# Kernel tuning notes

Measured on AMD Instinct MI355X. Metric: run time of the kernel, lower is better.

The kernel has to match this reference:

```python
import jax, jax.numpy as jnp
import numpy as np


def _conv1x1(x, w, b=None):
    # x: [B,C,H,W], w: [O,C]
    y = jnp.einsum('bchw,oc->bohw', x, w)
    if b is not None:
        y = y + b[None, :, None, None]
    return y


def _conv3x3_dilated(x, w, b, dil):
    p = dil  # padding == dilation keeps spatial size for 3x3 kernels
    y = jax.lax.conv_general_dilated(
        x, w, window_strides=(1, 1), padding=((p, p), (p, p)),
        rhs_dilation=(dil, dil), dimension_numbers=('NCHW', 'OIHW', 'NCHW'))
    return y + b[None, :, None, None]


def _upsample2x_align_corners(x):
    # bilinear, align_corners=True, scale factor 2
    B, C, H, W = x.shape
    oh, ow = 2 * H, 2 * W
    ys = jnp.linspace(0.0, H - 1.0, oh)
    xs = jnp.linspace(0.0, W - 1.0, ow)
    y0 = jnp.floor(ys).astype(jnp.int32)
    x0 = jnp.floor(xs).astype(jnp.int32)
    y1 = jnp.minimum(y0 + 1, H - 1)
    x1 = jnp.minimum(x0 + 1, W - 1)
    wy = (ys - y0)[None, None, :, None]
    wx = (xs - x0)[None, None, None, :]
    gt = x[:, :, y0, :]
    gb = x[:, :, y1, :]
    top = gt[:, :, :, x0] * (1 - wx) + gt[:, :, :, x1] * wx
    bot = gb[:, :, :, x0] * (1 - wx) + gb[:, :, :, x1] * wx
    return top * (1 - wy) + bot * wy


def _gr(ftr, ck_w, ck_b, avg_w, max_w, gcn_w):
    # GR module: attention-diagonal graph conv with degree normalization
    B, C, H, W = ftr.shape
    HW = H * W
    # ChannelAttention_diag -> diagonal entries cw: [B, M]
    avg = ftr.mean(axis=(2, 3))
    mx = ftr.max(axis=(2, 3))
    cw = jax.nn.sigmoid(jax.nn.relu(avg @ avg_w.T) + jax.nn.relu(mx @ max_w.T))  # [B,M]
    k = jax.nn.relu(_conv1x1(ftr, ck_w, ck_b)).reshape(B, -1, HW)  # [B,M,HW]
    q = jnp.swapaxes(k, 1, 2)  # [B,HW,M]
    # A = sigmoid(q @ diag(cw) @ k); degree d = rowsum(A)^(-1/2)
    A = jax.nn.sigmoid(jnp.einsum('bim,bm,bmj->bij', q, cw, k))  # [B,HW,HW]
    d = A.sum(axis=2) ** -0.5  # [B,HW]
    P = d[:, :, None] * q  # D^{-1/2} @ q, [B,HW,M]
    X = jnp.swapaxes(ftr.reshape(B, C, HW), 1, 2)  # [B,HW,C]
    PtX = jnp.einsum('bjm,bjc->bmc', P, X)  # [B,M,C]
    LX = X - jnp.einsum('bim,bmc->bic', P, cw[:, :, None] * PtX)
    Y = X + LX @ gcn_w  # GCN (no bias)
    return jnp.swapaxes(Y, 1, 2).reshape(B, C, H, W)


def setup_inputs() -> dict:
    key = jax.random.key(0)
    ks = jax.random.split(key, 20)
    B, C = 64, 1024
    Cq = C // 4  # 256
    Mi = Cq // 2  # 128, ChannelAttention inter channels
    s = 0.02
    inp = {
        'x_cur': jax.random.normal(ks[0], (B, C, 16, 16), jnp.float32),
        'x_lat': jax.random.normal(ks[1], (B, C, 8, 8), jnp.float32),
        'conv_w': jax.random.normal(ks[2], (Cq, C), jnp.float32) * s,
        'conv_b': jax.random.normal(ks[3], (Cq,), jnp.float32) * s,
        'conv1_w': jax.random.normal(ks[4], (C, Cq), jnp.float32) * s,
        'conv1_b': jax.random.normal(ks[5], (C,), jnp.float32) * s,
        'conv3_w': jax.random.normal(ks[6], (C, 3 * Cq), jnp.float32) * s,
        'conv3_b': jax.random.normal(ks[7], (C,), jnp.float32) * s,
        'rate0_w': jax.random.normal(ks[8], (Cq, C, 3, 3), jnp.float32) * s,
        'rate0_b': jax.random.normal(ks[9], (Cq,), jnp.float32) * s,
        'rate1_w': jax.random.normal(ks[10], (Cq, C, 3, 3), jnp.float32) * s,
        'rate1_b': jax.random.normal(ks[11], (Cq,), jnp.float32) * s,
        'rate2_w': jax.random.normal(ks[12], (Cq, C, 3, 3), jnp.float32) * s,
        'rate2_b': jax.random.normal(ks[13], (Cq,), jnp.float32) * s,
        'gr_ck_w': jax.random.normal(ks[14], (Mi, Cq), jnp.float32) * s,
        'gr_ck_b': jax.random.normal(ks[15], (Mi,), jnp.float32) * s,
        'gr_avg_w': jax.random.normal(ks[16], (Mi, Cq), jnp.float32) * s,
        'gr_max_w': jax.random.normal(ks[17], (Mi, Cq), jnp.float32) * s,
        'gr_gcn_w': jax.random.normal(ks[18], (Cq, Cq), jnp.float32) * s,
        'pre': 1,
    }
    return inp


def reference(x_cur, x_lat, conv_w, conv_b, conv1_w, conv1_b, conv3_w, conv3_b,
              rate0_w, rate0_b, rate1_w, rate1_b, rate2_w, rate2_b,
              gr_ck_w, gr_ck_b, gr_avg_w, gr_max_w, gr_gcn_w, pre):
    # pre == 1 path of Graph_aspp.forward
    gr_args = (gr_ck_w, gr_ck_b, gr_avg_w, gr_max_w, gr_gcn_w)
    x_sum = x_cur * _upsample2x_align_corners(x_lat) + x_cur
    f1 = _conv3x3_dilated(x_sum, rate0_w, rate0_b, 1) + _conv1x1(x_sum, conv_w, conv_b)
    x1 = _gr(f1, *gr_args)
    feature = _conv1x1(f1, conv1_w, conv1_b) + x_sum
    f2 = _conv3x3_dilated(feature, rate1_w, rate1_b, 2) + _conv1x1(feature, conv_w, conv_b)
    x2 = _gr(f2, *gr_args)
    feature = _conv1x1(f2, conv1_w, conv1_b) + x_sum
    f3 = _conv3x3_dilated(feature, rate2_w, rate2_b, 4) + _conv1x1(feature, conv_w, conv_b)
    x3 = _gr(f3, *gr_args)
    cat = jnp.concatenate((x1, x2, x3), axis=1)
    return _conv1x1(cat, conv3_w, conv3_b)
```

## Files before the change

### kernel.cpp

```cpp
#include <hip/hip_runtime.h>


typedef unsigned short ushort_t;
typedef unsigned int uint32;
typedef __attribute__((ext_vector_type(8))) unsigned short ushort8;
typedef __attribute__((ext_vector_type(8))) __bf16 bf16x8;
typedef __attribute__((ext_vector_type(4))) float f32x4;

__device__ __forceinline__ ushort_t f2b(float f) {
    union { float f; uint32 u; } v; v.f = f;
    uint32 r = v.u + 0x7fffu + ((v.u >> 16) & 1u);
    return (ushort_t)(r >> 16);
}
__device__ __forceinline__ float b2f(ushort_t b) {
    union { uint32 u; float f; } v; v.u = ((uint32)b) << 16;
    return v.f;
}
__device__ __forceinline__ float sigm(float x) { return 1.f / (1.f + __expf(-x)); }

__device__ __forceinline__ void gload_lds16(const void* g, void* l) {
    __builtin_amdgcn_global_load_lds(
        (__attribute__((address_space(1))) void*)g,
        (__attribute__((address_space(3))) void*)l, 16, 0, 0);
}

constexpr int EPI_RELU  = 1;
constexpr int EPI_FQ    = 2;
constexpr int EPI_SIG   = 3;
constexpr int EPI_XG    = 4;
constexpr int EPI_NEGCW = 5;
constexpr int EPI_Y     = 6;
constexpr int EPI_OUTT  = 7;

struct GemmP {
    const ushort_t* A; const ushort_t* B;
    const ushort_t* A2; const ushort_t* B2;
    long long aBatch, bBatch, a2Batch, b2Batch;
    int lda, ldb, lda2, ldb2;
    int Ksub, kSplit, dil;
    const float* bias;
    const ushort_t* res; long long resBatch; int ldres;
    ushort_t* obf; long long oBatch; int ldo;
    ushort_t* obf2;
    float* of32;
    const float* cw;
    const float* rscale;
    float* dsum;
    const ushort_t* zpage;
};

__device__ __forceinline__ void big_body(ushort_t* aT, ushort_t* bT,
                                         const GemmP& p, int bx, int by, int z) {
    const int tid = threadIdx.x;
    const int m0 = bx * 128, n0 = by * 128;
    const int lane = tid & 63, wid = tid >> 6;
    const int l15 = lane & 15, l16 = lane >> 4;
    const int wr = wid >> 1, wc = wid & 1;
    const int lrow = lane >> 3;
    const int sgran = (lane & 7) ^ lrow;

    int ayy[4], axx[4];
    const ushort_t* aBase[4];
    const ushort_t* bBase[4];
#pragma unroll
    for (int i = 0; i < 4; ++i) {
        int row = wid * 32 + i * 8 + lrow;
        int m = m0 + row;
        int bb = m >> 8;
        ayy[i] = (m >> 4) & 15; axx[i] = m & 15;
        aBase[i] = p.A + (long long)bb * 262144 + sgran * 8;
        bBase[i] = p.B + (long long)(n0 + row) * p.ldb + sgran * 8;
    }

    f32x4 acc[4][4];
#pragma unroll
    for (int i = 0; i < 4; ++i)
#pragma unroll
        for (int j = 0; j < 4; ++j) acc[i][j] = (f32x4){0.f, 0.f, 0.f, 0.f};

    const int gk0 = z * p.kSplit;
    const int ntap = p.Ksub >> 10;
    for (int ti = 0; ti < ntap; ++ti) {
        const int tap = (gk0 >> 10) + ti;
        int dy = 0, dx = 0;
        if (tap < 9) { int ky = tap / 3; dy = (ky - 1) * p.dil; dx = (tap - ky * 3 - 1) * p.dil; }
        const ushort_t* gaA[4];
        const ushort_t* gaB[4];
#pragma unroll
        for (int i = 0; i < 4; ++i) {
            int iy = ayy[i] + dy, ix = axx[i] + dx;
            bool ok = ((unsigned)iy < 16u) && ((unsigned)ix < 16u);
            gaA[i] = ok ? (aBase[i] + (((iy << 4) + ix) << 10)) : (p.zpage + sgran * 8);
            gaB[i] = bBase[i] + (tap << 10);
        }
        for (int kk = 0; kk < 16; ++kk) {
            const int kin = kk << 6;
#pragma unroll
            for (int i = 0; i < 4; ++i)
                gload_lds16(gaA[i] + kin, &aT[(wid * 32 + i * 8) * 64]);
#pragma unroll
            for (int i = 0; i < 4; ++i)
                gload_lds16(gaB[i] + kin, &bT[(wid * 32 + i * 8) * 64]);
            asm volatile("s_waitcnt vmcnt(0)" ::: "memory");
            __syncthreads();
#pragma unroll
            for (int ks = 0; ks < 2; ++ks) {
                bf16x8 af[4], bfr[4];
#pragma unroll
                for (int mi = 0; mi < 4; ++mi) {
                    int rr = wr * 64 + mi * 16 + l15;
                    int cc = (ks * 32 + l16 * 8) ^ ((rr & 7) << 3);
                    af[mi] = __builtin_bit_cast(bf16x8, *(const ushort8*)&aT[rr * 64 + cc]);
                }
#pragma unroll
                for (int ni = 0; ni < 4; ++ni) {
                    int rr = wc * 64 + ni * 16 + l15;
                    int cc = (ks * 32 + l16 * 8) ^ ((rr & 7) << 3);
                    bfr[ni] = __builtin_bit_cast(bf16x8, *(const ushort8*)&bT[rr * 64 + cc]);
                }
#pragma unroll
                for (int mi = 0; mi < 4; ++mi)
#pragma unroll
                    for (int ni = 0; ni < 4; ++ni)
                        acc[mi][ni] = __builtin_amdgcn_mfma_f32_16x16x32_bf16(af[mi], bfr[ni], acc[mi][ni], 0, 0, 0);
            }
            __syncthreads();
        }
    }
#pragma unroll
    for (int mi = 0; mi < 4; ++mi)
#pragma unroll
        for (int ni = 0; ni < 4; ++ni) {
            int gcol = n0 + wc * 64 + ni * 16 + l15;
            int growb = m0 + wr * 64 + mi * 16 + l16 * 4;
#pragma unroll
            for (int r = 0; r < 4; ++r)
                p.obf[(long long)z * p.oBatch + (long long)(growb + r) * 256 + gcol] =
                    f2b(acc[mi][ni][r]);
        }
}

template<int BM, int BN, int AMODE, int EPI>
__device__ __forceinline__ void gemm_body(ushort_t* aT, ushort_t* bT,
                                          const GemmP& p, int bx, int by, int z) {
    constexpr int APASS = BM / 32, BPASS = BN / 32;
    constexpr int MFRAG = BM / 32, NFRAG = BN / 32;
    const int tid = threadIdx.x;
    const int m0 = bx * BM, n0 = by * BN;
    const int lane = tid & 63, wid = tid >> 6;
    const int l15 = lane & 15, l16 = lane >> 4;
    const int wr = wid >> 1, wc = wid & 1;
    const int srow = tid >> 3, scol = (tid & 7) * 8;
    const int swcol = scol ^ ((srow & 7) << 3);

    const ushort_t* aptr[APASS];
    const ushort_t* bptr[BPASS];
    const ushort_t* aptr2[APASS];
    const ushort_t* bptr2[BPASS];
    float rsA[APASS];
#pragma unroll
    for (int pi = 0; pi < APASS; ++pi)
        aptr[pi] = p.A + (long long)z * p.aBatch +
                   (long long)(m0 + pi * 32 + srow) * p.lda + scol;
#pragma unroll
    for (int pi = 0; pi < BPASS; ++pi)
        bptr[pi] = p.B + (long long)z * p.bBatch +
                   (long long)(n0 + pi * 32 + srow) * p.ldb + scol;
    if constexpr (AMODE == 2) {
#pragma unroll
        for (int pi = 0; pi < APASS; ++pi) {
            aptr2[pi] = p.A2 + (long long)z * p.a2Batch +
                        (long long)(m0 + pi * 32 + srow) * p.lda2 + scol;
            rsA[pi] = p.rscale[z * 256 + m0 + pi * 32 + srow];
        }
#pragma unroll
        for (int pi = 0; pi < BPASS; ++pi)
            bptr2[pi] = p.B2 + (long long)z * p.b2Batch +
                        (long long)(n0 + pi * 32 + srow) * p.ldb2 + scol;
    }

    f32x4 acc[MFRAG][NFRAG];
#pragma unroll
    for (int i = 0; i < MFRAG; ++i)
#pragma unroll
        for (int j = 0; j < NFRAG; ++j) acc[i][j] = (f32x4){0.f, 0.f, 0.f, 0.f};

    ushort8 ar[APASS], br[BPASS];
    auto ldg = [&](int gk) {
        if (AMODE == 2 && gk >= 256) {
            int g2 = gk - 256;
#pragma unroll
            for (int pi = 0; pi < APASS; ++pi) {
                ushort8 t8 = *(const ushort8*)(aptr2[pi] + g2);
#pragma unroll
                for (int k = 0; k < 8; ++k) t8[k] = f2b(b2f(t8[k]) * rsA[pi]);
                ar[pi] = t8;
            }
#pragma unroll
            for (int pi = 0; pi < BPASS; ++pi) br[pi] = *(const ushort8*)(bptr2[pi] + g2);
        } else if constexpr (AMODE == 3) {
#pragma unroll
            for (int pi = 0; pi < APASS; ++pi) {
                ushort8 t8 = *(const ushort8*)(aptr[pi] + gk);
#pragma unroll
                for (int k = 0; k < 8; ++k)
                    t8[k] = f2b(b2f(t8[k]) * p.cw[(z << 7) + gk + scol + k]);
                ar[pi] = t8;
            }
#pragma unroll
            for (int pi = 0; pi < BPASS; ++pi) br[pi] = *(const ushort8*)(bptr[pi] + gk);
        } else {
#pragma unroll
            for (int pi = 0; pi < APASS; ++pi) ar[pi] = *(const ushort8*)(aptr[pi] + gk);
#pragma unroll
            for (int pi = 0; pi < BPASS; ++pi) br[pi] = *(const ushort8*)(bptr[pi] + gk);
        }
    };

    const int gk0 = z * p.kSplit;
    ldg(gk0);
    const int iters = p.Ksub >> 6;
    for (int it = 0; it < iters; ++it) {
#pragma unroll
        for (int pi = 0; pi < APASS; ++pi)
            *(ushort8*)&aT[(pi * 32 + srow) * 64 + swcol] = ar[pi];
#pragma unroll
        for (int pi = 0; pi < BPASS; ++pi)
            *(ushort8*)&bT[(pi * 32 + srow) * 64 + swcol] = br[pi];
        __syncthreads();
        if (it + 1 < iters) ldg(gk0 + (it + 1) * 64);
#pragma unroll
        for (int ks = 0; ks < 2; ++ks) {
            bf16x8 af[MFRAG], bfr[NFRAG];
#pragma unroll
            for (int mi = 0; mi < MFRAG; ++mi) {
                int rr = wr * (BM / 2) + mi * 16 + l15;
                int cc = (ks * 32 + l16 * 8) ^ ((rr & 7) << 3);
                af[mi] = __builtin_bit_cast(bf16x8, *(const ushort8*)&aT[rr * 64 + cc]);
            }
#pragma unroll
            for (int ni = 0; ni < NFRAG; ++ni) {
                int rr = wc * (BN / 2) + ni * 16 + l15;
                int cc = (ks * 32 + l16 * 8) ^ ((rr & 7) << 3);
                bfr[ni] = __builtin_bit_cast(bf16x8, *(const ushort8*)&bT[rr * 64 + cc]);
            }
#pragma unroll
            for (int mi = 0; mi < MFRAG; ++mi)
#pragma unroll
                for (int ni = 0; ni < NFRAG; ++ni)
                    acc[mi][ni] = __builtin_amdgcn_mfma_f32_16x16x32_bf16(af[mi], bfr[ni], acc[mi][ni], 0, 0, 0);
        }
        __syncthreads();
    }

#pragma unroll
    for (int mi = 0; mi < MFRAG; ++mi) {
        if constexpr (EPI == EPI_SIG) {
#pragma unroll
            for (int r = 0; r < 4; ++r) {
                float sv = 0.f;
#pragma unroll
                for (int ni = 0; ni < NFRAG; ++ni) sv += sigm(acc[mi][ni][r]);
                sv += __shfl_xor(sv, 1); sv += __shfl_xor(sv, 2);
                sv += __shfl_xor(sv, 4); sv += __shfl_xor(sv, 8);
                if (l15 == 0) {
                    int grow = m0 + wr * (BM / 2) + mi * 16 + l16 * 4 + r;
                    int q8 = by * 2 + wc;
                    p.dsum[q8 * 16384 + z * 256 + grow] = sv;
                }
            }
        } else {
#pragma unroll
            for (int ni = 0; ni < NFRAG; ++ni) {
                int gcol = n0 + wc * (BN / 2) + ni * 16 + l15;
                int growb = m0 + wr * (BM / 2) + mi * 16 + l16 * 4;
#pragma unroll
                for (int r = 0; r < 4; ++r) {
                    int grow = growb + r;
                    float v = acc[mi][ni][r];
                    if constexpr (EPI == EPI_RELU) {
                        v += p.bias[gcol]; v = fmaxf(v, 0.f);
                        p.obf[(long long)grow * p.ldo + gcol] = f2b(v);
                    } else if constexpr (EPI == EPI_FQ) {
                        v += p.bias[gcol];
                        if (gcol < 1024) {
                            v += b2f(p.res[(long long)grow * 1024 + gcol]);
                            p.obf[(long long)grow * 1024 + gcol] = f2b(v);
                        } else {
                            v = fmaxf(v, 0.f);
                            p.obf2[(long long)grow * 128 + (gcol - 1024)] = f2b(v);
                        }
                    } else if constexpr (EPI == EPI_XG) {
                        p.obf[(long long)z * p.oBatch + (long long)grow * p.ldo + gcol] = f2b(v);
                    } else if constexpr (EPI == EPI_NEGCW) {
                        v *= -p.cw[z * 128 + gcol];
                        p.obf[(long long)z * p.oBatch + (long long)grow * p.ldo + gcol] = f2b(v);
                    } else if constexpr (EPI == EPI_Y) {
                        v = b2f(p.res[(long long)z * p.resBatch + (long long)grow * p.ldres + gcol]) + v;
                        p.obf[(long long)z * p.oBatch + (long long)grow * p.ldo + gcol] = f2b(v);
                    } else if constexpr (EPI == EPI_OUTT) {
                        v += p.bias[grow];
                        int bb = gcol >> 8, px = gcol & 255;
                        p.of32[((long long)bb * 1024 + grow) * 256 + px] = v;
                    }
                }
            }
        }
    }
}

template<int BM, int BN, int AMODE, int EPI>
__global__ __launch_bounds__(256) void gemm_k(GemmP p) {
    __shared__ __align__(16) ushort_t aT[BM * 64];
    __shared__ __align__(16) ushort_t bT[BN * 64];
    gemm_body<BM, BN, AMODE, EPI>(aT, bT, p, blockIdx.x, blockIdx.y, blockIdx.z);
}

__device__ __forceinline__ void pool_body(void* lds, int b, const ushort_t* f,
                                          const float* aw, const float* mw,
                                          float* cw) {
    float* sa = (float*)lds;
    float* sm = sa + 256;
    int t = threadIdx.x;
    float s = 0.f, m = -3.4e38f;
    const ushort_t* base = f + (long long)b * 65536 + t;
    for (int px = 0; px < 256; ++px) { float v = b2f(base[px * 256]); s += v; m = fmaxf(m, v); }
    sa[t] = s * (1.f / 256.f);
    sm[t] = m;
    __syncthreads();
    if (t < 128) {
        float s1 = 0.f, s2 = 0.f;
        const float* a = aw + t * 256; const float* w = mw + t * 256;
        for (int c = 0; c < 256; ++c) { s1 += sa[c] * a[c]; s2 += sm[c] * w[c]; }
        s1 = fmaxf(s1, 0.f); s2 = fmaxf(s2, 0.f);
        cw[b * 128 + t] = sigm(s1 + s2);
    }
}

__device__ __forceinline__ void pscale_body(int jh, int b,
                                            const ushort_t* q, const float* dsum8,
                                            float* dscale, ushort_t* Pt) {
    __shared__ ushort_t t[128][130];
    __shared__ float dd[128];
    int j0 = jh * 128;
    int tid = threadIdx.x;
    if (tid < 128) {
        int pix = b * 256 + j0 + tid;
        float s = 0.f;
#pragma unroll
        for (int qs = 0; qs < 8; ++qs) s += dsum8[qs * 16384 + pix];
        float r = rsqrtf(s);
        dd[tid] = r;
        dscale[pix] = r;
    }
    __syncthreads();
    int jr = tid >> 7, m = tid & 127;
    for (int i = 0; i < 64; ++i) {
        int j = i * 2 + jr;
        long long qi = ((long long)(b * 256 + j0 + j)) * 128 + m;
        t[j][m] = f2b(dd[j] * b2f(q[qi]));
    }
    __syncthreads();
    for (int i = 0; i < 64; ++i) {
        int mm = i * 2 + jr;
        Pt[((long long)b << 15) + (mm << 8) + j0 + m] = t[m][mm];
    }
}

__global__ __launch_bounds__(256) void k_big_sig_y(GemmP pb, GemmP ps, GemmP px,
                                                   GemmP py) {
    __shared__ __align__(16) ushort_t lds[2 * 128 * 64];
    int z = blockIdx.z;
    if (z < 5) { big_body(lds, lds + 8192, pb, blockIdx.x, blockIdx.y, z); return; }
    if (z < 13) {
        int flat = (z - 5) * 256 + blockIdx.y * 128 + blockIdx.x;
        int bx = flat & 3, by = (flat >> 2) & 3, bz = flat >> 4;
        if (bz < 64) gemm_body<64, 64, 3, EPI_SIG>(lds, lds + 4096, ps, bx, by, bz);
        else         gemm_body<64, 64, 0, EPI_XG>(lds, lds + 4096, px, bx, by, bz - 64);
        return;
    }
    int flat = (z - 13) * 256 + blockIdx.y * 128 + blockIdx.x;
    gemm_body<64, 64, 2, EPI_Y>(lds, lds + 4096, py, flat & 3, (flat >> 2) & 3, flat >> 4);
}

__global__ __launch_bounds__(256) void k_fqpool_htn(GemmP pf, GemmP ph,
                                                    const float* aw, const float* mw,
                                                    float* cw) {
    __shared__ __align__(16) ushort_t lds[2 * 128 * 64];
    int y = blockIdx.y;
    if (y < 9) { gemm_body<128, 128, 0, EPI_FQ>(lds, lds + 8192, pf, blockIdx.x, y, 0); return; }
    if (y == 9) { if (blockIdx.x < 64) pool_body(lds, blockIdx.x, pf.A, aw, mw, cw); return; }
    int flat = (y - 10) * 128 + blockIdx.x;
    gemm_body<64, 64, 0, EPI_NEGCW>(lds, lds + 4096, ph, flat & 3, (flat >> 2) & 1, flat >> 3);
}

__global__ __launch_bounds__(256) void k_qpool_htn(GemmP pq, GemmP ph,
                                                   const float* aw, const float* mw,
                                                   float* cw) {
    __shared__ __align__(16) ushort_t lds[2 * 64 * 64];
    int y = blockIdx.y;
    if (y < 2) { gemm_body<64, 64, 0, EPI_RELU>(lds, lds + 4096, pq, blockIdx.x, y, 0); return; }
    if (y == 2) { if (blockIdx.x < 64) pool_body(lds, blockIdx.x, pq.A, aw, mw, cw); return; }
    int flat = (y - 3) * 256 + blockIdx.x;
    gemm_body<64, 64, 0, EPI_NEGCW>(lds, lds + 4096, ph, flat & 3, (flat >> 2) & 1, flat >> 3);
}

__global__ __launch_bounds__(256) void k_sigxg_y(GemmP ps, GemmP px, GemmP py) {
    __shared__ __align__(16) ushort_t aT[64 * 64];
    __shared__ __align__(16) ushort_t bT[64 * 64];
    int z = blockIdx.z;
    if (z < 64)       gemm_body<64, 64, 3, EPI_SIG>(aT, bT, ps, blockIdx.x, blockIdx.y, z);
    else if (z < 128) gemm_body<64, 64, 0, EPI_XG>(aT, bT, px, blockIdx.x, blockIdx.y, z - 64);
    else              gemm_body<64, 64, 2, EPI_Y>(aT, bT, py, blockIdx.x, blockIdx.y, z - 128);
}


__device__ __forceinline__ void combine_body(int bid, const ushort_t* t,
                                             const float* fbias_s, ushort_t* f) {
    int idx = bid * 256 + threadIdx.x;
    const long long N = 16384ll * 256;
    ushort8 a0 = *(const ushort8*)(t + (long long)idx * 8);
    ushort8 a1 = *(const ushort8*)(t + N + (long long)idx * 8);
    ushort8 a2 = *(const ushort8*)(t + 2 * N + (long long)idx * 8);
    ushort8 a3 = *(const ushort8*)(t + 3 * N + (long long)idx * 8);
    ushort8 a4 = *(const ushort8*)(t + 4 * N + (long long)idx * 8);
    int cb = (idx * 8) & 255;
    ushort8 o;
#pragma unroll
    for (int k = 0; k < 8; ++k)
        o[k] = f2b(b2f(a0[k]) + b2f(a1[k]) + b2f(a2[k]) + b2f(a3[k]) + b2f(a4[k]) + fbias_s[cb + k]);
    *(ushort8*)&f[(long long)idx * 8] = o;
}

__global__ void k_combine(const ushort_t* __restrict__ t, const float* __restrict__ fbias_s,
                          ushort_t* __restrict__ f) {
    combine_body(blockIdx.x, t, fbias_s, f);
}

__global__ __launch_bounds__(256) void k_comb_ps(const ushort_t* __restrict__ t,
                                                 const float* __restrict__ fbias_s,
                                                 ushort_t* __restrict__ f,
                                                 const ushort_t* __restrict__ q,
                                                 const float* __restrict__ dsum8,
                                                 float* __restrict__ dscale,
                                                 ushort_t* __restrict__ Pt) {
    int bid = blockIdx.x;
    if (bid < 2048) { combine_body(bid, t, fbias_s, f); return; }
    int pb = bid - 2048;
    pscale_body(pb & 1, pb >> 1, q, dsum8, dscale, Pt);
}

__global__ void k_upsum(const float* __restrict__ xc, const float* __restrict__ xl,
                        ushort_t* __restrict__ xs) {
    __shared__ float lat[64 * 64];
    __shared__ ushort_t tile[64 * 258];
    int b = blockIdx.x, c0 = blockIdx.y * 64;
    int t = threadIdx.x;
    for (int i = t; i < 4096; i += 256)
        lat[i] = xl[((long long)(b * 1024 + c0 + (i >> 6))) * 64 + (i & 63)];
    __syncthreads();
    int y = t >> 4, x = t & 15;
    float fy = y * (7.f / 15.f); int y0 = (int)fy; float wy = fy - y0; int y1 = y0 + 1 > 7 ? 7 : y0 + 1;
    float fx = x * (7.f / 15.f); int x0 = (int)fx; float wx = fx - x0; int x1 = x0 + 1 > 7 ? 7 : x0 + 1;
    for (int cc = 0; cc < 64; ++cc) {
        float cur = xc[((long long)(b * 1024 + c0 + cc)) * 256 + t];
        const float* L = &lat[cc * 64];
        float tv = L[y0 * 8 + x0] * (1.f - wx) + L[y0 * 8 + x1] * wx;
        float bv = L[y1 * 8 + x0] * (1.f - wx) + L[y1 * 8 + x1] * wx;
        float up = tv + (bv - tv) * wy;
        tile[cc * 258 + t] = f2b(cur * (1.f + up));
    }
    __syncthreads();
    for (int i = t; i < 16384; i += 256) {
        int px = i >> 6, cc = i & 63;
        xs[((long long)(b * 256 + px)) * 1024 + c0 + cc] = tile[cc * 258 + px];
    }
}

__global__ void k_pscale(const ushort_t* __restrict__ q, const float* __restrict__ dsum8,
                         float* __restrict__ dscale, ushort_t* __restrict__ Pt) {
    pscale_body(blockIdx.x, blockIdx.y, q, dsum8, dscale, Pt);
}

__global__ void k_packall(const float* r0, const float* r1, const float* r2,
                          const float* convw, const float* c1w, const float* c3w,
                          const float* ckw, const float* gcnw,
                          const float* rb0, const float* rb1, const float* rb2,
                          const float* cb, const float* c1b, const float* ckbias,
                          ushort_t* wbig3, ushort_t* wfq, ushort_t* w3b,
                          ushort_t* gcnT, float* fqbias, float* fbias,
                          ushort_t* zpage) {
    int blk = blockIdx.x, tid = threadIdx.x;
    if (blk < 768) {
        __shared__ float lw[10240];
        int s = blk >> 8, o = blk & 255;
        const float* rate = s == 0 ? r0 : (s == 1 ? r1 : r2);
        for (int i = tid; i < 9216; i += 256) lw[i] = rate[(long long)o * 9216 + i];
        for (int i = tid; i < 1024; i += 256) lw[9216 + i] = convw[(long long)o * 1024 + i];
        __syncthreads();
        ushort_t* dst = wbig3 + (long long)blk * 10240;
        for (int i = tid; i < 10240; i += 256) {
            int tap = i >> 10, ci = i & 1023;
            float v = (tap < 9) ? lw[ci * 9 + tap] : lw[9216 + ci];
            dst[i] = f2b(v);
        }
        return;
    }
    const int R1 = 262144;
    const int R2 = R1 + 32768;
    const int R3 = R2 + 786432;
    const int R4 = R3 + 65536;
    const int R5 = R4 + 1152;
    const int R6 = R5 + 768;
    const int R7 = R6 + 4096;
    int base = (blk - 768) * 2048 + tid * 8;
#pragma unroll
    for (int k = 0; k < 8; ++k) {
        int i = base + k;
        if (i >= R7) return;
        if (i < R1) wfq[i] = f2b(c1w[i]);
        else if (i < R2) wfq[i] = f2b(ckw[i - R1]);
        else if (i < R3) w3b[i - R2] = f2b(c3w[i - R2]);
        else if (i < R4) {
            int ii = i - R3; int c2 = ii >> 8, c1 = ii & 255;
            gcnT[ii] = f2b(gcnw[c1 * 256 + c2]);
        } else if (i < R5) {
            int ii = i - R4;
            fqbias[ii] = (ii < 1024) ? c1b[ii] : ckbias[ii - 1024];
        } else if (i < R6) {
            int ii = i - R5; int s = ii >> 8, t = ii & 255;
            const float* rb = s == 0 ? rb0 : (s == 1 ? rb1 : rb2);
            fbias[ii] = rb[t] + cb[t];
        } else {
            zpage[i - R6] = 0;
        }
    }
}

__global__ void k_sentinel(float* o, int n, float v) {
    int i = blockIdx.x * 256 + threadIdx.x; if (i < n) o[i] = v;
}

extern "C" void kernel_launch(void* const* d_in, const int* in_sizes, int n_in,
                              void* d_out, int out_size, void* d_ws, size_t ws_size,
                              hipStream_t stream) {
    const float* x_cur  = (const float*)d_in[0];
    const float* x_lat  = (const float*)d_in[1];
    const float* conv_w = (const float*)d_in[2];
    const float* conv_b = (const float*)d_in[3];
    const float* conv1_w = (const float*)d_in[4];
    const float* conv1_b = (const float*)d_in[5];
    const float* conv3_w = (const float*)d_in[6];
    const float* conv3_b = (const float*)d_in[7];
    const float* rate_w[3] = {(const float*)d_in[8], (const float*)d_in[10], (const float*)d_in[12]};
    const float* rate_b[3] = {(const float*)d_in[9], (const float*)d_in[11], (const float*)d_in[13]};
    const float* ck_w  = (const float*)d_in[14];
    const float* ck_b  = (const float*)d_in[15];
    const float* avg_w = (const float*)d_in[16];
    const float* max_w = (const float*)d_in[17];
    const float* gcn_w = (const float*)d_in[18];
    float* out = (float*)d_out;

    char* w = (char*)d_ws;
    auto take = [&](size_t bytes) { void* p = (void*)w; w += (bytes + 255) & ~(size_t)255; return p; };
    ushort_t* xsum   = (ushort_t*)take(16384ll * 1024 * 2);
    ushort_t* feat   = (ushort_t*)take(16384ll * 1024 * 2);
    ushort_t* fbufP[2];
    fbufP[0] = (ushort_t*)take(16384ll * 256 * 2);
    fbufP[1] = (ushort_t*)take(16384ll * 256 * 2);
    ushort_t* qbufP[2];
    qbufP[0] = (ushort_t*)take(16384ll * 128 * 2);
    qbufP[1] = (ushort_t*)take(16384ll * 128 * 2);
    ushort_t* xgt    = (ushort_t*)take(64ll * 256 * 256 * 2);
    ushort_t* Pt     = (ushort_t*)take(64ll * 128 * 256 * 2);
    ushort_t* Htn    = (ushort_t*)take(64ll * 256 * 128 * 2);
    ushort_t* wbig3  = (ushort_t*)take(3ll * 256 * 10240 * 2);
    ushort_t* wfq    = (ushort_t*)take(1152ll * 256 * 2);
    ushort_t* w3b    = (ushort_t*)take(1024ll * 768 * 2);
    ushort_t* gcnT   = (ushort_t*)take(256ll * 256 * 2);
    ushort_t* zpage  = (ushort_t*)take(8192);
    float*    fqbias = (float*)take(1152 * 4);
    float*    fbias  = (float*)take(3 * 256 * 4);
    float*    cwbP[2];
    cwbP[0] = (float*)take(64 * 128 * 4);
    cwbP[1] = (float*)take(64 * 128 * 4);
    float*    dscale = (float*)take(64 * 256 * 4);
    float*    dsum8  = (float*)take(8ll * 64 * 256 * 4);
    ushort_t* catb   = (ushort_t*)take(16384ll * 768 * 2);
    ushort_t* ftmp   = (ushort_t*)take(5ll * 16384 * 256 * 2);
    size_t need = (size_t)(w - (char*)d_ws);

    if (need > ws_size) {
        float v = 1.0e6f + (float)(ws_size >> 20);
        k_sentinel<<<(out_size + 255) / 256, 256, 0, stream>>>(out, out_size, v);
        return;
    }

    auto PBIG = [&](int s) {
        GemmP p{};
        p.A = (s == 0) ? xsum : feat;
        p.B = wbig3 + (long long)s * 256 * 10240; p.ldb = 10240;
        p.Ksub = 2048; p.kSplit = 2048; p.dil = 1 << s;
        p.obf = ftmp; p.oBatch = 16384ll * 256;
        p.zpage = zpage;
        return p;
    };
    auto PSIG = [&](int s) {
        GemmP p{};
        p.A = qbufP[s & 1]; p.aBatch = 32768; p.lda = 128;
        p.B = qbufP[s & 1]; p.bBatch = 32768; p.ldb = 128;
        p.Ksub = 128; p.dsum = dsum8; p.cw = cwbP[s & 1];
        return p;
    };
    auto PXG = [&](int s) {
        GemmP p{};
        p.A = gcnT; p.aBatch = 0;            p.lda = 256;
        p.B = fbufP[s & 1]; p.bBatch = 65536; p.ldb = 256;
        p.Ksub = 256;
        p.obf = xgt; p.oBatch = 65536; p.ldo = 256;
        return p;
    };
    auto PHTN = [&](int s) {
        GemmP p{};
        p.A = xgt; p.aBatch = 65536; p.lda = 256;
        p.B = Pt;  p.bBatch = 32768; p.ldb = 256;
        p.Ksub = 256; p.cw = cwbP[s & 1];
        p.obf = Htn; p.oBatch = 32768; p.ldo = 128;
        return p;
    };
    auto PY = [&](int s) {
        GemmP p{};
        p.A = fbufP[s & 1]; p.aBatch = 65536; p.lda = 256;
        p.B = gcnT; p.bBatch = 0;             p.ldb = 256;
        p.A2 = qbufP[s & 1]; p.a2Batch = 32768; p.lda2 = 128; p.rscale = dscale;
        p.B2 = Htn;          p.b2Batch = 32768; p.ldb2 = 128;
        p.Ksub = 384;
        p.res = fbufP[s & 1]; p.resBatch = 65536; p.ldres = 256;
        p.obf = catb + s * 256; p.oBatch = 256ll * 768; p.ldo = 768;
        return p;
    };
    auto PFQ = [&](int s) {
        GemmP p{};
        p.A = fbufP[s & 1]; p.lda = 256; p.B = wfq; p.ldb = 256;
        p.Ksub = 256; p.bias = fqbias;
        p.res = xsum;
        p.obf = feat; p.obf2 = qbufP[s & 1];
        return p;
    };
    GemmP pz{};

    k_packall<<<768 + 563, 256, 0, stream>>>(
        rate_w[0], rate_w[1], rate_w[2], conv_w, conv1_w, conv3_w, ck_w, gcn_w,
        rate_b[0], rate_b[1], rate_b[2], conv_b, conv1_b, ck_b,
        wbig3, wfq, w3b, gcnT, fqbias, fbias, zpage);
    k_upsum<<<dim3(64, 16), 256, 0, stream>>>(x_cur, x_lat, xsum);

    k_big_sig_y<<<dim3(128, 2, 5), 256, 0, stream>>>(PBIG(0), pz, pz, pz);
    k_combine<<<2048, 256, 0, stream>>>(ftmp, fbias + 0 * 256, fbufP[0]);
    k_fqpool_htn<<<dim3(128, 10), 256, 0, stream>>>(PFQ(0), pz, avg_w, max_w, cwbP[0]);
    k_big_sig_y<<<dim3(128, 2, 13), 256, 0, stream>>>(PBIG(1), PSIG(0), PXG(0), pz);
    k_comb_ps<<<2048 + 128, 256, 0, stream>>>(ftmp, fbias + 1 * 256, fbufP[1],
                                              qbufP[0], dsum8, dscale, Pt);
    k_fqpool_htn<<<dim3(128, 14), 256, 0, stream>>>(PFQ(1), PHTN(0), avg_w, max_w, cwbP[1]);
    k_big_sig_y<<<dim3(128, 2, 17), 256, 0, stream>>>(PBIG(2), PSIG(1), PXG(1), PY(0));
    k_comb_ps<<<2048 + 128, 256, 0, stream>>>(ftmp, fbias + 2 * 256, fbufP[0],
                                              qbufP[1], dsum8, dscale, Pt);
    {
        GemmP pq{};
        pq.A = fbufP[0]; pq.lda = 256; pq.B = wfq + 1024 * 256; pq.ldb = 256;
        pq.Ksub = 256;
        pq.bias = ck_b; pq.obf = qbufP[0]; pq.ldo = 128;
        k_qpool_htn<<<dim3(256, 5), 256, 0, stream>>>(pq, PHTN(1), avg_w, max_w, cwbP[0]);
    }
    k_sigxg_y<<<dim3(4, 4, 192), 256, 0, stream>>>(PSIG(2), PXG(2), PY(1));
    k_pscale<<<dim3(2, 64), 256, 0, stream>>>(qbufP[0], dsum8, dscale, Pt);
    gemm_k<64, 64, 0, EPI_NEGCW><<<dim3(4, 2, 64), 256, 0, stream>>>(PHTN(2));
    gemm_k<64, 64, 2, EPI_Y><<<dim3(4, 4, 64), 256, 0, stream>>>(PY(2));
    {
        GemmP p{};
        p.A = w3b;  p.lda = 768;
        p.B = catb; p.ldb = 768;
        p.Ksub = 768; p.bias = conv3_b; p.of32 = out;
        gemm_k<128, 128, 0, EPI_OUTT><<<dim3(8, 128, 1), 256, 0, stream>>>(p);
    }
}
```

Baseline: 630.0 us.

## Merge weight packing and upsample-sum into one launch; raise MFMA wave priority

The weight-packing kernel and the upsample-multiply-sum kernel become one grid. Extra blocks run the upsum body out of a shared-memory buffer, which removes a kernel launch and lets the two independent jobs overlap. The shared buffer is now the larger of the two needs, about 48KB, so every block in the merged grid carries that allocation and this may reduce occupancy for the packing blocks. Separately, s_setprio is raised around the MFMA inner loop of a GEMM to favour waves that are issuing matrix instructions.

```diff
diff --git a/kernel.cpp b/kernel.cpp
--- a/kernel.cpp
+++ b/kernel.cpp
@@ -118,11 +118,13 @@
                     int cc = (ks * 32 + l16 * 8) ^ ((rr & 7) << 3);
                     bfr[ni] = __builtin_bit_cast(bf16x8, *(const ushort8*)&bT[rr * 64 + cc]);
                 }
+                __builtin_amdgcn_s_setprio(1);
 #pragma unroll
                 for (int mi = 0; mi < 4; ++mi)
 #pragma unroll
                     for (int ni = 0; ni < 4; ++ni)
                         acc[mi][ni] = __builtin_amdgcn_mfma_f32_16x16x32_bf16(af[mi], bfr[ni], acc[mi][ni], 0, 0, 0);
+                __builtin_amdgcn_s_setprio(0);
             }
             __syncthreads();
         }
@@ -450,11 +452,11 @@
     pscale_body(pb & 1, pb >> 1, q, dsum8, dscale, Pt);
 }
 
-__global__ void k_upsum(const float* __restrict__ xc, const float* __restrict__ xl,
-                        ushort_t* __restrict__ xs) {
-    __shared__ float lat[64 * 64];
-    __shared__ ushort_t tile[64 * 258];
-    int b = blockIdx.x, c0 = blockIdx.y * 64;
+__device__ __forceinline__ void upsum_body(void* smem, int b, int c0,
+                                           const float* xc, const float* xl,
+                                           ushort_t* xs) {
+    float* lat = (float*)smem;
+    ushort_t* tile = (ushort_t*)((char*)smem + 16384);
     int t = threadIdx.x;
     for (int i = t; i < 4096; i += 256)
         lat[i] = xl[((long long)(b * 1024 + c0 + (i >> 6))) * 64 + (i & 63)];
@@ -482,17 +484,24 @@
     pscale_body(blockIdx.x, blockIdx.y, q, dsum8, dscale, Pt);
 }
 
-__global__ void k_packall(const float* r0, const float* r1, const float* r2,
-                          const float* convw, const float* c1w, const float* c3w,
-                          const float* ckw, const float* gcnw,
-                          const float* rb0, const float* rb1, const float* rb2,
-                          const float* cb, const float* c1b, const float* ckbias,
-                          ushort_t* wbig3, ushort_t* wfq, ushort_t* w3b,
-                          ushort_t* gcnT, float* fqbias, float* fbias,
-                          ushort_t* zpage) {
+__global__ __launch_bounds__(256) void k_packup(
+    const float* r0, const float* r1, const float* r2,
+    const float* convw, const float* c1w, const float* c3w,
+    const float* ckw, const float* gcnw,
+    const float* rb0, const float* rb1, const float* rb2,
+    const float* cb, const float* c1b, const float* ckbias,
+    ushort_t* wbig3, ushort_t* wfq, ushort_t* w3b,
+    ushort_t* gcnT, float* fqbias, float* fbias, ushort_t* zpage,
+    const float* x_cur, const float* x_lat, ushort_t* xsum) {
+    __shared__ __align__(16) char smem[49408];
     int blk = blockIdx.x, tid = threadIdx.x;
+    if (blk >= 1331) {
+        int u = blk - 1331;
+        upsum_body(smem, u & 63, (u >> 6) * 64, x_cur, x_lat, xsum);
+        return;
+    }
     if (blk < 768) {
-        __shared__ float lw[10240];
+        float* lw = (float*)smem;
         int s = blk >> 8, o = blk & 255;
         const float* rate = s == 0 ? r0 : (s == 1 ? r1 : r2);
         for (int i = tid; i < 9216; i += 256) lw[i] = rate[(long long)o * 9216 + i];
@@ -649,11 +658,11 @@
     };
     GemmP pz{};
 
-    k_packall<<<768 + 563, 256, 0, stream>>>(
+    k_packup<<<768 + 563 + 1024, 256, 0, stream>>>(
         rate_w[0], rate_w[1], rate_w[2], conv_w, conv1_w, conv3_w, ck_w, gcn_w,
         rate_b[0], rate_b[1], rate_b[2], conv_b, conv1_b, ck_b,
-        wbig3, wfq, w3b, gcnT, fqbias, fbias, zpage);
-    k_upsum<<<dim3(64, 16), 256, 0, stream>>>(x_cur, x_lat, xsum);
+        wbig3, wfq, w3b, gcnT, fqbias, fbias, zpage,
+        x_cur, x_lat, xsum);
 
     k_big_sig_y<<<dim3(128, 2, 5), 256, 0, stream>>>(PBIG(0), pz, pz, pz);
     k_combine<<<2048, 256, 0, stream>>>(ftmp, fbias + 0 * 256, fbufP[0]);
```

Result: no change. 623.0 us, median of 3 (-1.1%).
